# Kernel optimization log

Hardware: AMD Instinct MI355X
Metric: run time of the kernel (lower is better)

The kernel has to match this reference:

```python
import jax, jax.numpy as jnp
import numpy as np

SCALE_BASE = 512.0
GAMMA = 0.96875


def _rotate_every_two(x):
    x1 = x[..., ::2]
    x2 = x[..., 1::2]
    return jnp.stack([-x2, x1], axis=-1).reshape(x.shape)


def _dup_interleave(m):
    # [L, d/2] -> [L, d], each column duplicated: (a,b) -> (a,a,b,b)
    return jnp.repeat(m, 2, axis=-1)


def _xpos(x, downscale=False):
    # x: [B, L, d]; offset = 0 (parallel form)
    B, L, d = x.shape
    half = d // 2
    pos = jnp.arange(L, dtype=x.dtype)
    # xpos per-channel scale base
    sv = (jnp.arange(0, d, 2, dtype=x.dtype) + 0.4 * d) / (1.4 * d)   # [d/2]
    scale = sv[None, :] ** (pos[:, None] / SCALE_BASE)                 # [L, d/2]
    if downscale:
        scale = 1.0 / scale
    inv_freq = 1.0 / (10000.0 ** (jnp.arange(half, dtype=x.dtype) / half))
    sinusoid = pos[:, None] * inv_freq[None, :]                        # [L, d/2]
    sin = _dup_interleave(jnp.sin(sinusoid) * scale)                   # [L, d]
    cos = _dup_interleave(jnp.cos(sinusoid) * scale)                   # [L, d]
    return x * cos[None] + _rotate_every_two(x) * sin[None]


def _get_D(seq_len, dtype):
    idx = jnp.arange(seq_len)
    diff = idx[:, None] - idx[None, :]                                 # n - m
    safe = jnp.where(diff >= 0, diff, 0).astype(dtype)
    return jnp.where(diff >= 0, GAMMA ** safe, jnp.zeros((), dtype))   # [L, L]


def setup_inputs() -> dict:
    key = jax.random.key(0)
    k1, k2, k3, k4 = jax.random.split(key, 4)
    B, L, H, D = 2, 4096, 1024, 64
    X = jax.random.normal(k1, (B, L, H), dtype=jnp.float32)
    W_Q = jax.random.normal(k2, (H, D), dtype=jnp.float32) / H
    W_K = jax.random.normal(k3, (H, D), dtype=jnp.float32) / H
    W_V = jax.random.normal(k4, (H, D), dtype=jnp.float32) / H
    return {"X": X, "W_Q": W_Q, "W_K": W_K, "W_V": W_V}


def reference(X, W_Q, W_K, W_V):
    L = X.shape[1]
    Dmask = _get_D(L, X.dtype)                     # [L, L]
    Q = _xpos(X @ W_Q)                             # [B, L, d]
    K = _xpos(X @ W_K, downscale=True)             # [B, L, d]
    V = X @ W_V                                    # [B, L, v]
    ret = jnp.einsum('bnd,bmd->bnm', Q, K) * Dmask[None]  # [B, L, L]
    return ret @ V                                 # [B, L, v]
```

## Files before the change

kernel.cpp:

```cpp
#include <hip/hip_runtime.h>
#include <math.h>

#define NB 2
#define LL 4096
#define HH 1024
#define DD 64
#define CHK 64
#define NCH 64
#define BLROWS (NB*LL)
#define NCHT (NB*NCH)
#define GAMMA 0.96875f

typedef _Float16 f16x8 __attribute__((ext_vector_type(8)));
typedef _Float16 f16x4 __attribute__((ext_vector_type(4)));
typedef float    f32x4 __attribute__((ext_vector_type(4)));

#define WCH 12288
#define SBS 584

__global__ __launch_bounds__(256) void prep_w(
    const float* __restrict__ WQ, const float* __restrict__ WK,
    const float* __restrict__ WV, _Float16* __restrict__ Wf)
{
    const unsigned t = blockIdx.x * 256 + threadIdx.x;
    const unsigned kchunk = t / 1536u;
    const unsigned s = t - kchunk * 1536u;
    const int ct2  = s >> 6;
    const int lane = s & 63;
    const int n16  = ct2 >> 1;
    const int kt   = ct2 & 1;
    const int quad = lane >> 4;
    const int n    = n16 * 16 + (lane & 15);
    const int k0   = (int)kchunk * 64 + kt * 32 + quad * 8;
    const int m    = n >> 6;
    const int d    = n & 63;
    const float* Wm = (m == 0) ? WQ : (m == 1) ? WK : WV;
    f16x8 hv;
#pragma unroll
    for (int j = 0; j < 8; ++j)
        hv[j] = (_Float16)(Wm[(size_t)(k0 + j) * DD + d] * 1024.f);
    *(f16x8*)&Wf[(size_t)t * 8] = hv;
}

__global__ __launch_bounds__(256) void proj_mfma(
    const float* __restrict__ X, const _Float16* __restrict__ Wf,
    _Float16* __restrict__ Qr, _Float16* __restrict__ Kf,
    _Float16* __restrict__ Vf)
{
    const int tid  = threadIdx.x;
    const int wv   = tid >> 6;
    const int lane = tid & 63;
    const int quad = lane >> 4;
    const int l15  = lane & 15;
    const int rg   = blockIdx.x;
    const size_t xrow = (size_t)(rg * 16 + l15) * HH;

    f32x4 acc[3];
#pragma unroll
    for (int i = 0; i < 3; ++i) acc[i] = (f32x4){0.f, 0.f, 0.f, 0.f};

    float4 pA[4];
    f16x8  pB[6];
    {
        const float* xp = &X[xrow + quad * 8];
        pA[0] = *(const float4*)&xp[0];
        pA[1] = *(const float4*)&xp[4];
        pA[2] = *(const float4*)&xp[32];
        pA[3] = *(const float4*)&xp[36];
#pragma unroll
        for (int cj = 0; cj < 3; ++cj)
#pragma unroll
            for (int kt = 0; kt < 2; ++kt)
                pB[cj * 2 + kt] = *(const f16x8*)&Wf[
                    (size_t)((((wv * 3 + cj) * 2 + kt) * 64 + lane)) * 8];
    }

    for (int ch = 0; ch < 16; ++ch) {
        f16x8 a[2];
#pragma unroll
        for (int kt = 0; kt < 2; ++kt) {
            const float4 xa = pA[kt * 2], xb = pA[kt * 2 + 1];
            a[kt][0] = (_Float16)xa.x; a[kt][1] = (_Float16)xa.y;
            a[kt][2] = (_Float16)xa.z; a[kt][3] = (_Float16)xa.w;
            a[kt][4] = (_Float16)xb.x; a[kt][5] = (_Float16)xb.y;
            a[kt][6] = (_Float16)xb.z; a[kt][7] = (_Float16)xb.w;
        }
        f16x8 b[6];
#pragma unroll
        for (int i = 0; i < 6; ++i) b[i] = pB[i];

        if (ch + 1 < 16) {
            const float* xp = &X[xrow + (ch + 1) * 64 + quad * 8];
            pA[0] = *(const float4*)&xp[0];
            pA[1] = *(const float4*)&xp[4];
            pA[2] = *(const float4*)&xp[32];
            pA[3] = *(const float4*)&xp[36];
            const size_t cb = (size_t)(ch + 1) * WCH;
#pragma unroll
            for (int cj = 0; cj < 3; ++cj)
#pragma unroll
                for (int kt = 0; kt < 2; ++kt)
                    pB[cj * 2 + kt] = *(const f16x8*)&Wf[cb +
                        (size_t)((((wv * 3 + cj) * 2 + kt) * 64 + lane)) * 8];
        }
#pragma unroll
        for (int kt = 0; kt < 2; ++kt)
#pragma unroll
            for (int cj = 0; cj < 3; ++cj)
                acc[cj] = __builtin_amdgcn_mfma_f32_16x16x32_f16(
                    a[kt], b[cj * 2 + kt], acc[cj], 0, 0, 0);
    }

#pragma unroll
    for (int cj = 0; cj < 3; ++cj) {
        const int ctg = wv * 3 + cj;
        const f32x4 v = acc[cj];
        const int col = ctg * 16 + l15;
        const int mat = ctg >> 2;
        const int d   = col & 63;
        if (mat < 2) {
            const int i2 = d >> 1;
            const float sv   = (2.f * (float)i2 + 25.6f) / 89.6f;
            const float l2sv = log2f(sv);
            const float ifr  = exp2f(-13.28771237954945f * ((float)i2 / 32.f));
            const float sgn  = (mat == 0) ? 1.f : -1.f;
#pragma unroll
            for (int r = 0; r < 4; ++r) {
                const int row = rg * 16 + quad * 4 + r;
                const float val = v[r] * (1.f / 1024.f);
                const float p = __shfl_xor(val, 1, 64);
                const float pf  = (float)(row & (LL - 1));
                const float pfs = (float)(row & 63);
                const float scl = exp2f(sgn * (pfs * (1.f / 512.f)) * l2sv);
                float s, c;
                sincosf(pf * ifr, &s, &c);
                s *= scl; c *= scl;
                const float o = ((col & 1) == 0) ? val * c - p * s
                                                 : val * c + p * s;
                if (mat == 0) {
                    Qr[(size_t)row * DD + d] = (_Float16)o;
                } else {
                    const int b2 = row >> 12, posb = row & 4095;
                    Kf[(((size_t)b2 * 8 + (d >> 3)) * 4096 + posb) * 8 + (d & 7)] =
                        (_Float16)o;
                }
            }
        } else {
            f16x4 vv;
#pragma unroll
            for (int r = 0; r < 4; ++r) vv[r] = (_Float16)(v[r] * (1.f / 1024.f));
            const int row0 = rg * 16 + quad * 4;
            const int b2 = row0 >> 12, posb = row0 & 4095;
            *(f16x4*)&Vf[(((size_t)b2 * 512 + (posb >> 3)) * 64 + d) * 8 + (posb & 7)] = vv;
        }
    }
}

__global__ __launch_bounds__(256) void chunk_out(
    const _Float16* __restrict__ Qr, const _Float16* __restrict__ Kf,
    const _Float16* __restrict__ Vf, float* __restrict__ out)
{
    __shared__ __align__(16) unsigned char smraw[20032];
    _Float16* Sb  = (_Float16*)smraw;
    _Float16* svp = (_Float16*)(smraw + 18688);
    float*    pwl = (float*)(smraw + 19712);

    const int tid   = threadIdx.x;
    const int bc    = blockIdx.x;
    const int chunk = bc >> 2;
    const int qt    = bc & 3;
    const int w     = tid >> 6;
    const int lane  = tid & 63;
    const int quad  = lane >> 4;
    const int l15   = lane & 15;
    const int cloc  = chunk & 63;
    const int bB    = chunk >> 6;
    const size_t rowbase = (size_t)chunk * CHK + qt * 16;
    const float l2g = log2f(GAMMA);

    if (tid < 65) pwl[tid] = exp2f((float)tid * l2g);
#pragma unroll
    for (int e = 0; e < 2; ++e) {
        const int idx = tid + e * 256;
        const int dl  = (idx >> 6) + 1;
        const int dd  = idx & 63;
        const float sv = (2.f * (float)(dd >> 1) + 25.6f) / 89.6f;
        svp[idx] = (_Float16)exp2f(0.125f * (float)dl * log2f(sv));
    }

    f16x8 aQ[2];
#pragma unroll
    for (int ks = 0; ks < 2; ++ks)
        aQ[ks] = *(const f16x8*)&Qr[(rowbase + l15) * DD + ks * 32 + quad * 8];
    __syncthreads();

    {
        const int posb = cloc * 64 + w * 16 + l15;
        f32x4 sA = (f32x4){0.f, 0.f, 0.f, 0.f};
#pragma unroll
        for (int ks = 0; ks < 2; ++ks) {
            const f16x8 bK = *(const f16x8*)&Kf[(((size_t)bB * 8 + ks * 4 + quad)
                                                * 4096 + posb) * 8];
            sA = __builtin_amdgcn_mfma_f32_16x16x32_f16(aQ[ks], bK, sA, 0, 0, 0);
        }
        const int m = w * 16 + l15;
#pragma unroll
        for (int r = 0; r < 4; ++r) {
            const int nl = quad * 4 + r;
            const int n64 = qt * 16 + nl;
            const float val = (n64 >= m) ? sA[r] * pwl[n64 - m] : 0.f;
            Sb[nl * SBS + m] = (_Float16)val;
        }
    }

    for (int jc = w; jc < 32; jc += 4) {
        const int dlt = 8 - (jc >> 2);
        const bool valid = (dlt <= cloc);
        const int mq = (jc * 16 + l15) & 63;
        const float gl = valid ? exp2f((float)(64 * dlt - mq) * l2g) : 0.f;
        const _Float16 glh = (_Float16)gl;
        const int cs = valid ? (chunk - dlt) : chunk;
        const int posb = (cs & 63) * 64 + mq;
        f32x4 sc4 = (f32x4){0.f, 0.f, 0.f, 0.f};
#pragma unroll
        for (int ks = 0; ks < 2; ++ks) {
            const f16x8 bk = *(const f16x8*)&Kf[(((size_t)bB * 8 + ks * 4 + quad)
                                                * 4096 + posb) * 8];
            const f16x8 sv8 = *(const f16x8*)&svp[(dlt - 1) * 64 + ks * 32 + quad * 8];
            f16x8 b2;
#pragma unroll
            for (int j = 0; j < 8; ++j) b2[j] = bk[j] * glh * sv8[j];
            sc4 = __builtin_amdgcn_mfma_f32_16x16x32_f16(aQ[ks], b2, sc4, 0, 0, 0);
        }
#pragma unroll
        for (int r = 0; r < 4; ++r) {
            const int nl = quad * 4 + r;
            const int na = qt * 16 + nl;
            Sb[nl * SBS + 64 + jc * 16 + l15] = (_Float16)(sc4[r] * pwl[na]);
        }
    }
    __syncthreads();

    f32x4 oA = (f32x4){0.f, 0.f, 0.f, 0.f};
    const int dp = w * 16 + l15;
    for (int ks5 = 0; ks5 < 18; ++ks5) {
        const f16x8 aS = *(const f16x8*)&Sb[l15 * SBS + ks5 * 32 + quad * 8];
        const int m0 = ks5 * 32 + quad * 8;
        int gr;
        if (ks5 < 2) {
            gr = chunk * 64 + m0;
        } else {
            const int mc = m0 - 64;
            int cs2 = chunk - 8 + (mc >> 6);
            if (cs2 < (chunk & ~63)) cs2 = chunk;
            gr = cs2 * 64 + (mc & 63);
        }
        const int b2 = gr >> 12, pb = gr & 4095;
        const size_t vb = ((size_t)b2 * 512 + (pb >> 3)) * 64;
        const f16x8 bV = *(const f16x8*)&Vf[(vb + dp) * 8];
        oA = __builtin_amdgcn_mfma_f32_16x16x32_f16(aS, bV, oA, 0, 0, 0);
    }
#pragma unroll
    for (int r = 0; r < 4; ++r)
        out[(rowbase + quad * 4 + r) * DD + dp] = oA[r];
}

extern "C" void kernel_launch(void* const* d_in, const int* in_sizes, int n_in,
                              void* d_out, int out_size, void* d_ws, size_t ws_size,
                              hipStream_t stream)
{
    const float* X  = (const float*)d_in[0];
    const float* WQ = (const float*)d_in[1];
    const float* WK = (const float*)d_in[2];
    const float* WV = (const float*)d_in[3];
    float* outp = (float*)d_out;

    _Float16* Wf = (_Float16*)d_ws;
    _Float16* Qr = Wf + 196608;
    _Float16* Kf = Qr + (size_t)BLROWS * DD;
    _Float16* Vf = Kf + (size_t)BLROWS * DD;

    hipLaunchKernelGGL(prep_w, dim3(96), dim3(256), 0, stream,
                       WQ, WK, WV, Wf);
    hipLaunchKernelGGL(proj_mfma, dim3(512), dim3(256), 0, stream,
                       X, Wf, Qr, Kf, Vf);
    hipLaunchKernelGGL(chunk_out, dim3(512), dim3(256), 0, stream,
                       Qr, Kf, Vf, outp);
}
```

Before: 106.9 us.

## Precompute xPos rotary tables and process two row tiles per projection block

The weight-prep kernel gains extra blocks that fill per-position cos/sin tables, already multiplied by the xPos scale, for Q and K. The projection epilogue now reads these tables instead of calling sincosf, exp2f and log2f per element. Each projection block now handles 32 rows, with two MFMA accumulator sets sharing the same weight fragments, so weight loads are reused and the grid is halved. This costs more registers and extra table traffic, and the chunk_out V loop is fully unrolled.

Measured after the change: 105.5 us (median of 2 runs). Within noise of the previous version (-1.4%).

```diff
diff --git a/kernel.cpp b/kernel.cpp
--- a/kernel.cpp
+++ b/kernel.cpp
@@ -20,30 +20,49 @@
 
 __global__ __launch_bounds__(256) void prep_w(
     const float* __restrict__ WQ, const float* __restrict__ WK,
-    const float* __restrict__ WV, _Float16* __restrict__ Wf)
+    const float* __restrict__ WV, _Float16* __restrict__ Wf,
+    float2* __restrict__ tabQ, float2* __restrict__ tabK)
 {
-    const unsigned t = blockIdx.x * 256 + threadIdx.x;
-    const unsigned kchunk = t / 1536u;
-    const unsigned s = t - kchunk * 1536u;
-    const int ct2  = s >> 6;
-    const int lane = s & 63;
-    const int n16  = ct2 >> 1;
-    const int kt   = ct2 & 1;
-    const int quad = lane >> 4;
-    const int n    = n16 * 16 + (lane & 15);
-    const int k0   = (int)kchunk * 64 + kt * 32 + quad * 8;
-    const int m    = n >> 6;
-    const int d    = n & 63;
-    const float* Wm = (m == 0) ? WQ : (m == 1) ? WK : WV;
-    f16x8 hv;
-#pragma unroll
-    for (int j = 0; j < 8; ++j)
-        hv[j] = (_Float16)(Wm[(size_t)(k0 + j) * DD + d] * 1024.f);
-    *(f16x8*)&Wf[(size_t)t * 8] = hv;
+    const unsigned tid = threadIdx.x;
+    if (blockIdx.x < 96) {
+        const unsigned t = blockIdx.x * 256 + tid;
+        const unsigned kchunk = t / 1536u;
+        const unsigned s = t - kchunk * 1536u;
+        const int ct2  = s >> 6;
+        const int lane = s & 63;
+        const int n16  = ct2 >> 1;
+        const int kt   = ct2 & 1;
+        const int quad = lane >> 4;
+        const int n    = n16 * 16 + (lane & 15);
+        const int k0   = (int)kchunk * 64 + kt * 32 + quad * 8;
+        const int m    = n >> 6;
+        const int d    = n & 63;
+        const float* Wm = (m == 0) ? WQ : (m == 1) ? WK : WV;
+        f16x8 hv;
+#pragma unroll
+        for (int j = 0; j < 8; ++j)
+            hv[j] = (_Float16)(Wm[(size_t)(k0 + j) * DD + d] * 1024.f);
+        *(f16x8*)&Wf[(size_t)t * 8] = hv;
+    } else {
+        const unsigned t2 = (blockIdx.x - 96) * 256 + tid;
+        const int i2  = (int)(t2 >> 12);
+        const int pos = (int)(t2 & 4095u);
+        const float ifr = exp2f(-13.28771237954945f * ((float)i2 / 32.f));
+        float sn, cn;
+        sincosf((float)pos * ifr, &sn, &cn);
+        const float sv   = (2.f * (float)i2 + 25.6f) / 89.6f;
+        const float l2sv = log2f(sv);
+        const float arg  = ((float)(pos & 63) * (1.f / 512.f)) * l2sv;
+        const float sq = exp2f(arg);
+        const float sk = exp2f(-arg);
+        tabQ[t2] = make_float2(cn * sq, sn * sq);
+        tabK[t2] = make_float2(cn * sk, sn * sk);
+    }
 }
 
 __global__ __launch_bounds__(256) void proj_mfma(
     const float* __restrict__ X, const _Float16* __restrict__ Wf,
+    const float2* __restrict__ tabQ, const float2* __restrict__ tabK,
     _Float16* __restrict__ Qr, _Float16* __restrict__ Kf,
     _Float16* __restrict__ Vf)
 {
@@ -53,20 +72,28 @@
     const int quad = lane >> 4;
     const int l15  = lane & 15;
     const int rg   = blockIdx.x;
-    const size_t xrow = (size_t)(rg * 16 + l15) * HH;
-
-    f32x4 acc[3];
-#pragma unroll
-    for (int i = 0; i < 3; ++i) acc[i] = (f32x4){0.f, 0.f, 0.f, 0.f};
-
-    float4 pA[4];
+    const size_t xrow0 = (size_t)(rg * 32 + l15) * HH;
+    const size_t xrow1 = xrow0 + (size_t)16 * HH;
+
+    f32x4 acc[2][3];
+#pragma unroll
+    for (int s = 0; s < 2; ++s)
+#pragma unroll
+        for (int i = 0; i < 3; ++i) acc[s][i] = (f32x4){0.f, 0.f, 0.f, 0.f};
+
+    float4 pA[2][4];
     f16x8  pB[6];
     {
-        const float* xp = &X[xrow + quad * 8];
-        pA[0] = *(const float4*)&xp[0];
-        pA[1] = *(const float4*)&xp[4];
-        pA[2] = *(const float4*)&xp[32];
-        pA[3] = *(const float4*)&xp[36];
+        const float* xp0 = &X[xrow0 + quad * 8];
+        const float* xp1 = &X[xrow1 + quad * 8];
+        pA[0][0] = *(const float4*)&xp0[0];
+        pA[0][1] = *(const float4*)&xp0[4];
+        pA[0][2] = *(const float4*)&xp0[32];
+        pA[0][3] = *(const float4*)&xp0[36];
+        pA[1][0] = *(const float4*)&xp1[0];
+        pA[1][1] = *(const float4*)&xp1[4];
+        pA[1][2] = *(const float4*)&xp1[32];
+        pA[1][3] = *(const float4*)&xp1[36];
 #pragma unroll
         for (int cj = 0; cj < 3; ++cj)
 #pragma unroll
@@ -76,25 +103,32 @@
     }
 
     for (int ch = 0; ch < 16; ++ch) {
-        f16x8 a[2];
-#pragma unroll
-        for (int kt = 0; kt < 2; ++kt) {
-            const float4 xa = pA[kt * 2], xb = pA[kt * 2 + 1];
-            a[kt][0] = (_Float16)xa.x; a[kt][1] = (_Float16)xa.y;
-            a[kt][2] = (_Float16)xa.z; a[kt][3] = (_Float16)xa.w;
-            a[kt][4] = (_Float16)xb.x; a[kt][5] = (_Float16)xb.y;
-            a[kt][6] = (_Float16)xb.z; a[kt][7] = (_Float16)xb.w;
-        }
+        f16x8 a[2][2];
+#pragma unroll
+        for (int s = 0; s < 2; ++s)
+#pragma unroll
+            for (int kt = 0; kt < 2; ++kt) {
+                const float4 xa = pA[s][kt * 2], xb = pA[s][kt * 2 + 1];
+                a[s][kt][0] = (_Float16)xa.x; a[s][kt][1] = (_Float16)xa.y;
+                a[s][kt][2] = (_Float16)xa.z; a[s][kt][3] = (_Float16)xa.w;
+                a[s][kt][4] = (_Float16)xb.x; a[s][kt][5] = (_Float16)xb.y;
+                a[s][kt][6] = (_Float16)xb.z; a[s][kt][7] = (_Float16)xb.w;
+            }
         f16x8 b[6];
 #pragma unroll
         for (int i = 0; i < 6; ++i) b[i] = pB[i];
 
         if (ch + 1 < 16) {
-            const float* xp = &X[xrow + (ch + 1) * 64 + quad * 8];
-            pA[0] = *(const float4*)&xp[0];
-            pA[1] = *(const float4*)&xp[4];
-            pA[2] = *(const float4*)&xp[32];
-            pA[3] = *(const float4*)&xp[36];
+            const float* xp0 = &X[xrow0 + (ch + 1) * 64 + quad * 8];
+            const float* xp1 = &X[xrow1 + (ch + 1) * 64 + quad * 8];
+            pA[0][0] = *(const float4*)&xp0[0];
+            pA[0][1] = *(const float4*)&xp0[4];
+            pA[0][2] = *(const float4*)&xp0[32];
+            pA[0][3] = *(const float4*)&xp0[36];
+            pA[1][0] = *(const float4*)&xp1[0];
+            pA[1][1] = *(const float4*)&xp1[4];
+            pA[1][2] = *(const float4*)&xp1[32];
+            pA[1][3] = *(const float4*)&xp1[36];
             const size_t cb = (size_t)(ch + 1) * WCH;
 #pragma unroll
             for (int cj = 0; cj < 3; ++cj)
@@ -107,51 +141,54 @@
         for (int kt = 0; kt < 2; ++kt)
 #pragma unroll
             for (int cj = 0; cj < 3; ++cj)
-                acc[cj] = __builtin_amdgcn_mfma_f32_16x16x32_f16(
-                    a[kt], b[cj * 2 + kt], acc[cj], 0, 0, 0);
-    }
-
-#pragma unroll
-    for (int cj = 0; cj < 3; ++cj) {
-        const int ctg = wv * 3 + cj;
-        const f32x4 v = acc[cj];
-        const int col = ctg * 16 + l15;
-        const int mat = ctg >> 2;
-        const int d   = col & 63;
-        if (mat < 2) {
-            const int i2 = d >> 1;
-            const float sv   = (2.f * (float)i2 + 25.6f) / 89.6f;
-            const float l2sv = log2f(sv);
-            const float ifr  = exp2f(-13.28771237954945f * ((float)i2 / 32.f));
-            const float sgn  = (mat == 0) ? 1.f : -1.f;
-#pragma unroll
-            for (int r = 0; r < 4; ++r) {
-                const int row = rg * 16 + quad * 4 + r;
-                const float val = v[r] * (1.f / 1024.f);
-                const float p = __shfl_xor(val, 1, 64);
-                const float pf  = (float)(row & (LL - 1));
-                const float pfs = (float)(row & 63);
-                const float scl = exp2f(sgn * (pfs * (1.f / 512.f)) * l2sv);
-                float s, c;
-                sincosf(pf * ifr, &s, &c);
-                s *= scl; c *= scl;
-                const float o = ((col & 1) == 0) ? val * c - p * s
-                                                 : val * c + p * s;
-                if (mat == 0) {
-                    Qr[(size_t)row * DD + d] = (_Float16)o;
-                } else {
-                    const int b2 = row >> 12, posb = row & 4095;
-                    Kf[(((size_t)b2 * 8 + (d >> 3)) * 4096 + posb) * 8 + (d & 7)] =
-                        (_Float16)o;
+#pragma unroll
+                for (int s = 0; s < 2; ++s)
+                    acc[s][cj] = __builtin_amdgcn_mfma_f32_16x16x32_f16(
+                        a[s][kt], b[cj * 2 + kt], acc[s][cj], 0, 0, 0);
+    }
+
+#pragma unroll
+    for (int s = 0; s < 2; ++s) {
+        const int rowq = rg * 32 + s * 16 + quad * 4;
+#pragma unroll
+        for (int cj = 0; cj < 3; ++cj) {
+            const int ctg = wv * 3 + cj;
+            const f32x4 v = acc[s][cj];
+            const int col = ctg * 16 + l15;
+            const int mat = ctg >> 2;
+            const int d   = col & 63;
+            if (mat < 2) {
+                const int i2 = d >> 1;
+                const float2* tab = (mat == 0) ? tabQ : tabK;
+                const float2* tp = tab + ((size_t)i2 << 12) + (rowq & (LL - 1));
+                const float4 cs01 = *(const float4*)tp;
+                const float4 cs23 = *(const float4*)(tp + 2);
+#pragma unroll
+                for (int r = 0; r < 4; ++r) {
+                    const int row = rowq + r;
+                    const float val = v[r] * (1.f / 1024.f);
+                    const float p = __shfl_xor(val, 1, 64);
+                    const float cc = (r == 0) ? cs01.x : (r == 1) ? cs01.z
+                                   : (r == 2) ? cs23.x : cs23.z;
+                    const float ss = (r == 0) ? cs01.y : (r == 1) ? cs01.w
+                                   : (r == 2) ? cs23.y : cs23.w;
+                    const float o = ((col & 1) == 0) ? val * cc - p * ss
+                                                     : val * cc + p * ss;
+                    if (mat == 0) {
+                        Qr[(size_t)row * DD + d] = (_Float16)o;
+                    } else {
+                        const int b2 = row >> 12, posb = row & 4095;
+                        Kf[(((size_t)b2 * 8 + (d >> 3)) * 4096 + posb) * 8 + (d & 7)] =
+                            (_Float16)o;
+                    }
                 }
+            } else {
+                f16x4 vv;
+#pragma unroll
+                for (int r = 0; r < 4; ++r) vv[r] = (_Float16)(v[r] * (1.f / 1024.f));
+                const int b2 = rowq >> 12, posb = rowq & 4095;
+                *(f16x4*)&Vf[(((size_t)b2 * 512 + (posb >> 3)) * 64 + d) * 8 + (posb & 7)] = vv;
             }
-        } else {
-            f16x4 vv;
-#pragma unroll
-            for (int r = 0; r < 4; ++r) vv[r] = (_Float16)(v[r] * (1.f / 1024.f));
-            const int row0 = rg * 16 + quad * 4;
-            const int b2 = row0 >> 12, posb = row0 & 4095;
-            *(f16x4*)&Vf[(((size_t)b2 * 512 + (posb >> 3)) * 64 + d) * 8 + (posb & 7)] = vv;
         }
     }
 }
@@ -243,6 +280,8 @@
 
     f32x4 oA = (f32x4){0.f, 0.f, 0.f, 0.f};
     const int dp = w * 16 + l15;
+    const int chunkbase = chunk & ~63;
+#pragma unroll
     for (int ks5 = 0; ks5 < 18; ++ks5) {
         const f16x8 aS = *(const f16x8*)&Sb[l15 * SBS + ks5 * 32 + quad * 8];
         const int m0 = ks5 * 32 + quad * 8;
@@ -252,7 +291,7 @@
         } else {
             const int mc = m0 - 64;
             int cs2 = chunk - 8 + (mc >> 6);
-            if (cs2 < (chunk & ~63)) cs2 = chunk;
+            cs2 = (cs2 < chunkbase) ? chunk : cs2;
             gr = cs2 * 64 + (mc & 63);
         }
         const int b2 = gr >> 12, pb = gr & 4095;
@@ -279,11 +318,13 @@
     _Float16* Qr = Wf + 196608;
     _Float16* Kf = Qr + (size_t)BLROWS * DD;
     _Float16* Vf = Kf + (size_t)BLROWS * DD;
-
-    hipLaunchKernelGGL(prep_w, dim3(96), dim3(256), 0, stream,
-                       WQ, WK, WV, Wf);
-    hipLaunchKernelGGL(proj_mfma, dim3(512), dim3(256), 0, stream,
-                       X, Wf, Qr, Kf, Vf);
+    float2* tabQ = (float2*)(Vf + (size_t)BLROWS * DD);
+    float2* tabK = tabQ + 131072;
+
+    hipLaunchKernelGGL(prep_w, dim3(608), dim3(256), 0, stream,
+                       WQ, WK, WV, Wf, tabQ, tabK);
+    hipLaunchKernelGGL(proj_mfma, dim3(256), dim3(256), 0, stream,
+                       X, Wf, tabQ, tabK, Qr, Kf, Vf);
     hipLaunchKernelGGL(chunk_out, dim3(512), dim3(256), 0, stream,
                        Qr, Kf, Vf, outp);
 }
```
